# Optimization experiments

Measured on AMD Instinct MI355X. Metric: run time of the kernel, lower is better.

Reference implementation:

```python
import jax, jax.numpy as jnp
import numpy as np
from jax import lax

LIDAR_MAX_X = 30.0
LIDAR_MAX_Y = 30.0


def bilinear_sample(value, grid):
    """value: (bs,C,H,W); grid: (bs,nq,np,2) in [-1,1] -> (bs,C,nq,np)."""
    bs, C, H, W = value.shape
    _, nq, npts, _ = grid.shape
    gx = (grid[..., 0] + 1.0) / 2.0 * (W - 1)
    gy = (grid[..., 1] + 1.0) / 2.0 * (H - 1)
    # torch .long() truncates; in-bounds coords are non-negative so trunc == floor
    x0 = jnp.clip(gx.astype(jnp.int32), 0, W - 2)
    y0 = jnp.clip(gy.astype(jnp.int32), 0, H - 2)
    x1 = x0 + 1
    y1 = y0 + 1
    wx = jnp.clip(gx - x0.astype(gx.dtype), 0.0, 1.0).reshape(bs, 1, -1)
    wy = jnp.clip(gy - y0.astype(gy.dtype), 0.0, 1.0).reshape(bs, 1, -1)
    x0f = x0.reshape(bs, -1); x1f = x1.reshape(bs, -1)
    y0f = y0.reshape(bs, -1); y1f = y1.reshape(bs, -1)
    vflat = value.reshape(bs, C, H * W)
    gather = jax.vmap(lambda v, i: v[:, i])  # (C,HW),(N,) -> (C,N)
    v00 = gather(vflat, y0f * W + x0f)
    v01 = gather(vflat, y0f * W + x1f)
    v10 = gather(vflat, y1f * W + x0f)
    v11 = gather(vflat, y1f * W + x1f)
    sampled = (v00 * (1 - wx) * (1 - wy) + v01 * wx * (1 - wy)
               + v10 * (1 - wx) * wy + v11 * wx * wy)
    sampled = sampled.reshape(bs, C, nq, npts)
    gx0, gy0 = grid[..., 0], grid[..., 1]
    in_bounds = ((gx0 >= -1) & (gx0 <= 1) & (gy0 >= -1) & (gy0 <= 1))
    return sampled * in_bounds[:, None].astype(sampled.dtype)


def setup_inputs() -> dict:
    key = jax.random.key(0)
    ks = jax.random.split(key, 8)
    bs, nq, npts = 8, 2048, 8
    C_in, H, W = 64, 200, 200
    D = 256
    queries = jax.random.normal(ks[0], (bs, nq, D), dtype=jnp.float32)
    # lidar-frame waypoints, mostly in-bounds
    traj_points = jax.random.uniform(ks[1], (bs, nq, npts, 2), jnp.float32, -30.0, 30.0)
    bev_feature = jax.random.normal(ks[2], (bs, C_in, H, W), dtype=jnp.float32)
    attn_w = jax.random.normal(ks[3], (npts, D), dtype=jnp.float32) * 0.05
    attn_b = jnp.zeros((npts,), jnp.float32)
    out_w = jax.random.normal(ks[4], (D, D), dtype=jnp.float32) * (1.0 / np.sqrt(D))
    out_b = jnp.zeros((D,), jnp.float32)
    conv_w = jax.random.normal(ks[5], (D, C_in, 3, 3), dtype=jnp.float32) * 0.05
    conv_b = jnp.zeros((D,), jnp.float32)
    return {"queries": queries, "traj_points": traj_points, "bev_feature": bev_feature,
            "attn_w": attn_w, "attn_b": attn_b, "out_w": out_w, "out_b": out_b,
            "conv_w": conv_w, "conv_b": conv_b}


def reference(queries, traj_points, bev_feature, attn_w, attn_b, out_w, out_b, conv_w, conv_b):
    # normalize trajectory and swap (x,y) -> (y,x)
    norm = traj_points / jnp.array([LIDAR_MAX_Y, LIDAR_MAX_X], dtype=traj_points.dtype)
    grid = norm[..., ::-1]  # (bs,nq,np,2)
    # per-point attention weights
    attw = jax.nn.softmax(jnp.einsum('bqd,pd->bqp', queries, attn_w) + attn_b, axis=-1)
    # value projection: Conv3x3 + ReLU
    value = lax.conv_general_dilated(bev_feature, conv_w, (1, 1), ((1, 1), (1, 1)),
                                     dimension_numbers=('NCHW', 'OIHW', 'NCHW'))
    value = jax.nn.relu(value + conv_b[None, :, None, None])
    sampled = lax.stop_gradient(bilinear_sample(value, grid))  # (bs,C,nq,np)
    out = jnp.einsum('bcqp,bqp->bqc', sampled, attw)  # weighted sum over points
    out = jnp.einsum('bqc,dc->bqd', out, out_w) + out_b
    return out + queries  # dropout is identity in eval mode
```

## Files before the change

kernel.cpp:

```cpp
#include <hip/hip_runtime.h>

typedef unsigned short u16;
typedef _Float16 f16x8 __attribute__((ext_vector_type(8)));
typedef _Float16 f16x2 __attribute__((ext_vector_type(2)));
typedef float f32x4 __attribute__((ext_vector_type(4)));

__device__ __forceinline__ u16 f2h(float f){
  _Float16 h = (_Float16)f;
  return __builtin_bit_cast(u16, h);
}

__device__ __forceinline__ void load_lds16(const void* g, void* l){
  __builtin_amdgcn_global_load_lds((const __attribute__((address_space(1))) void*)g,
                                   (__attribute__((address_space(3))) void*)l,
                                   16, 0, 0);
}

__global__ __launch_bounds__(256) void kv5_transpose(const float* __restrict__ bev,
                                                     u16* __restrict__ bevT)
{
  __shared__ float t[64][65];
  const int tid = threadIdx.x;
  const int bid = blockIdx.x;
  const int wc = bid & 3;
  const int h  = (bid >> 2) % 200;
  const int b  = bid / 800;
  const int w0 = wc << 6;

  const int wl = (tid & 15) << 2;
  const int cb = tid >> 4;
  if (w0 + wl < 200){
    #pragma unroll
    for (int r = 0; r < 4; ++r){
      const int c = cb + (r << 4);
      const float4 v = *(const float4*)&bev[(((size_t)b*64 + c)*200 + h)*200 + (w0 + wl)];
      t[c][wl] = v.x; t[c][wl+1] = v.y; t[c][wl+2] = v.z; t[c][wl+3] = v.w;
    }
  }
  __syncthreads();
  const int c0 = (tid & 7) << 3;
  #pragma unroll
  for (int j = 0; j < 2; ++j){
    const int wl2 = (tid >> 3) + (j << 5);
    if (w0 + wl2 < 200){
      unsigned r0 = (unsigned)f2h(t[c0+0][wl2]) | ((unsigned)f2h(t[c0+1][wl2]) << 16);
      unsigned r1 = (unsigned)f2h(t[c0+2][wl2]) | ((unsigned)f2h(t[c0+3][wl2]) << 16);
      unsigned r2 = (unsigned)f2h(t[c0+4][wl2]) | ((unsigned)f2h(t[c0+5][wl2]) << 16);
      unsigned r3 = (unsigned)f2h(t[c0+6][wl2]) | ((unsigned)f2h(t[c0+7][wl2]) << 16);
      uint4 o = {r0, r1, r2, r3};
      *(uint4*)&bevT[(((size_t)b*202 + h + 1)*202 + (w0 + wl2 + 1))*64 + c0] = o;
    }
  }
}

__global__ __launch_bounds__(256) void kv5_prep(const float* __restrict__ conv_w,
                                                const float* __restrict__ out_w,
                                                u16* __restrict__ Wr,
                                                u16* __restrict__ owb)
{
  const int i = blockIdx.x * 256 + threadIdx.x;
  if (i < 9*256*64){
    const int t9 = i / (256*64);
    const int rem = i - t9*(256*64);
    const int d = rem >> 6, c = rem & 63;
    Wr[i] = f2h(conv_w[(size_t)(d*64 + c)*9 + t9]);
  } else {
    const int j = i - 9*256*64;
    if (j < 65536) owb[j] = f2h(out_w[j]);
  }
}

__global__ __launch_bounds__(256) void kv5_attw(const float* __restrict__ q,
                                                const float* __restrict__ aw,
                                                const float* __restrict__ ab,
                                                float* __restrict__ attw)
{
  const int lane = threadIdx.x & 63;
  const int bq = blockIdx.x * 4 + (threadIdx.x >> 6);
  const float4 qv = *(const float4*)&q[(size_t)bq*256 + (lane << 2)];
  float lg[8];
  #pragma unroll
  for (int p = 0; p < 8; ++p){
    const float4 wv = *(const float4*)&aw[p*256 + (lane << 2)];
    float d = qv.x*wv.x + qv.y*wv.y + qv.z*wv.z + qv.w*wv.w;
    #pragma unroll
    for (int off = 32; off > 0; off >>= 1) d += __shfl_xor(d, off);
    lg[p] = d + ab[p];
  }
  float mx = lg[0];
  #pragma unroll
  for (int p = 1; p < 8; ++p) mx = fmaxf(mx, lg[p]);
  float sum = 0.f;
  #pragma unroll
  for (int p = 0; p < 8; ++p){ lg[p] = expf(lg[p] - mx); sum += lg[p]; }
  const float inv = 1.f / sum;
  if (lane == 0){
    float4 o0 = {lg[0]*inv, lg[1]*inv, lg[2]*inv, lg[3]*inv};
    float4 o1 = {lg[4]*inv, lg[5]*inv, lg[6]*inv, lg[7]*inv};
    *(float4*)&attw[(size_t)bq*8]     = o0;
    *(float4*)&attw[(size_t)bq*8 + 4] = o1;
  }
}

__global__ __launch_bounds__(256) void kv5_conv(const u16* __restrict__ bevT,
                                                const u16* __restrict__ Wr,
                                                const float* __restrict__ conv_b,
                                                u16* __restrict__ value)
{
  __shared__ __align__(16) u16 lds[32768];
  const int tid  = threadIdx.x;
  const int bid  = blockIdx.x;
  const int n0   = (bid & 1) << 7;
  const int m0   = (bid >> 1) << 7;
  const int lane = tid & 63;
  const int wv   = tid >> 6;
  const int wm   = (wv >> 1) << 6;
  const int wn   = (wv & 1) << 6;
  const int c0   = (((tid & 7) ^ ((tid >> 3) & 7)) << 3);

  int baseA[4], baseB[4];
  #pragma unroll
  for (int i = 0; i < 4; ++i){
    const int m = m0 + (i << 5) + (tid >> 3);
    const int b = m / 40000;
    const int pix = m - b * 40000;
    const int h = pix / 200;
    const int w = pix - h * 200;
    baseA[i] = ((b*202 + h)*202 + w)*64 + c0;
    baseB[i] = (n0 + (i << 5) + (tid >> 3))*64 + c0;
  }

#define STAGE_TAP(dbuf, t9) do{                                            \
    const int ky_ = (t9)/3;                                                \
    const int offA_ = (ky_*202 + ((t9) - ky_*3))*64;                       \
    const u16* wsrc_ = Wr + (t9)*16384;                                    \
    for (int i_ = 0; i_ < 4; ++i_){                                        \
      load_lds16(bevT + baseA[i_] + offA_,                                 \
                 lds + (dbuf)*16384 + (i_ << 11) + (wv << 9));             \
      load_lds16(wsrc_ + baseB[i_],                                        \
                 lds + (dbuf)*16384 + 8192 + (i_ << 11) + (wv << 9));      \
    } }while(0)

  const f32x4 z = {0.f, 0.f, 0.f, 0.f};
  f32x4 acc[4][4];
  #pragma unroll
  for (int mf = 0; mf < 4; ++mf)
    #pragma unroll
    for (int nf = 0; nf < 4; ++nf)
      acc[mf][nf] = z;

  STAGE_TAP(0, 0);
  __syncthreads();

  int cur = 0;
  for (int t9 = 0; t9 < 9; ++t9){
    if (t9 < 8) STAGE_TAP(cur ^ 1, t9 + 1);

    const int rbase = cur << 14;
    const int swz = lane & 7;
    f16x8 a_frag[2][4], b_frag[2][4];
    #pragma unroll
    for (int kh = 0; kh < 2; ++kh){
      const int c16 = (((kh << 2) + (lane >> 4)) ^ swz) << 3;
      #pragma unroll
      for (int f = 0; f < 4; ++f){
        a_frag[kh][f] = *(const f16x8*)&lds[rbase + (wm + (f << 4) + (lane & 15))*64 + c16];
        b_frag[kh][f] = *(const f16x8*)&lds[rbase + 8192 + (wn + (f << 4) + (lane & 15))*64 + c16];
      }
    }
    #pragma unroll
    for (int kh = 0; kh < 2; ++kh)
      #pragma unroll
      for (int mf = 0; mf < 4; ++mf)
        #pragma unroll
        for (int nf = 0; nf < 4; ++nf)
          acc[mf][nf] = __builtin_amdgcn_mfma_f32_16x16x32_f16(a_frag[kh][mf], b_frag[kh][nf], acc[mf][nf], 0, 0, 0);

    __syncthreads();
    cur ^= 1;
  }
#undef STAGE_TAP

  #pragma unroll
  for (int nf = 0; nf < 4; ++nf){
    const int col = wn + (nf << 4) + (lane & 15);
    const float bias = conv_b[n0 + col];
    #pragma unroll
    for (int mf = 0; mf < 4; ++mf)
      #pragma unroll
      for (int rr = 0; rr < 4; ++rr){
        const int row = wm + (mf << 4) + ((lane >> 4) << 2) + rr;
        lds[row*128 + col] = f2h(fmaxf(acc[mf][nf][rr] + bias, 0.f));
      }
  }
  __syncthreads();
  #pragma unroll
  for (int it = 0; it < 8; ++it){
    const int idx = (it << 8) + tid;
    const int row = idx >> 4;
    const int ce  = (idx & 15) << 3;
    const f32x4 v = *(const f32x4*)&lds[row*128 + ce];
    *(f32x4*)&value[(size_t)(m0 + row)*256 + n0 + ce] = v;
  }
}

__global__ __launch_bounds__(256) void kv5_sample(const float* __restrict__ traj,
                                                  const float* __restrict__ attw,
                                                  const u16* __restrict__ value,
                                                  u16* __restrict__ sbh)
{
  __shared__ int   pixs[2][32];
  __shared__ float wgts[2][32];
  const int tid  = threadIdx.x;
  const int half = tid >> 7;
  const int t    = tid & 127;
  const int q    = (blockIdx.x << 1) + half;

  if (t < 8){
    const int p = t;
    const float ty = traj[((size_t)q*8 + p)*2 + 0];
    const float tx = traj[((size_t)q*8 + p)*2 + 1];
    float aw = attw[q*8 + p];
    const float gxn = tx / 30.f;
    const float gyn = ty / 30.f;
    if (!(gxn >= -1.f && gxn <= 1.f && gyn >= -1.f && gyn <= 1.f)) aw = 0.f;
    const float gx = (gxn + 1.f) * 0.5f * 199.f;
    const float gy = (gyn + 1.f) * 0.5f * 199.f;
    int x0 = (int)gx; x0 = min(max(x0, 0), 198);
    int y0 = (int)gy; y0 = min(max(y0, 0), 198);
    const float wx = fminf(fmaxf(gx - (float)x0, 0.f), 1.f);
    const float wy = fminf(fmaxf(gy - (float)y0, 0.f), 1.f);
    const int base = y0*200 + x0;
    pixs[half][p*4+0] = base;       wgts[half][p*4+0] = aw*(1.f-wx)*(1.f-wy);
    pixs[half][p*4+1] = base+1;     wgts[half][p*4+1] = aw*wx*(1.f-wy);
    pixs[half][p*4+2] = base+200;   wgts[half][p*4+2] = aw*(1.f-wx)*wy;
    pixs[half][p*4+3] = base+201;   wgts[half][p*4+3] = aw*wx*wy;
  }
  __syncthreads();
  const size_t vbase = (size_t)(q >> 11) * 40000;
  float a0 = 0.f, a1 = 0.f;
  #pragma unroll
  for (int i = 0; i < 32; ++i){
    const float w = wgts[half][i];
    const f16x2 pv = *(const f16x2*)&value[((vbase + pixs[half][i]) << 8) + (t << 1)];
    a0 = fmaf(w, (float)pv.x, a0);
    a1 = fmaf(w, (float)pv.y, a1);
  }
  const unsigned o = (unsigned)f2h(a0) | ((unsigned)f2h(a1) << 16);
  *(unsigned*)&sbh[((size_t)q << 8) + (t << 1)] = o;
}

__global__ __launch_bounds__(256) void kv5_outgemm(const u16* __restrict__ sbh,
                                                   const u16* __restrict__ owb,
                                                   const float* __restrict__ out_b,
                                                   const float* __restrict__ queries,
                                                   float* __restrict__ outp)
{
  __shared__ __align__(16) u16 lds[16384];
  const int tid  = threadIdx.x;
  const int bid  = blockIdx.x;
  const int n0   = (bid & 1) << 7;
  const int m0   = (bid >> 1) << 7;
  const int lane = tid & 63;
  const int wv   = tid >> 6;
  const int wm   = (wv >> 1) << 6;
  const int wn   = (wv & 1) << 6;
  const int c0   = (tid & 7) << 3;

  int baseA[4], baseB[4];
  #pragma unroll
  for (int i = 0; i < 4; ++i){
    baseA[i] = (m0 + (i << 5) + (tid >> 3))*256 + c0;
    baseB[i] = (n0 + (i << 5) + (tid >> 3))*256 + c0;
  }
  const f32x4 z = {0.f, 0.f, 0.f, 0.f};
  f32x4 acc[4][4];
  #pragma unroll
  for (int mf = 0; mf < 4; ++mf)
    #pragma unroll
    for (int nf = 0; nf < 4; ++nf)
      acc[mf][nf] = z;

  for (int kk = 0; kk < 4; ++kk){
    #pragma unroll
    for (int i = 0; i < 4; ++i){
      load_lds16(sbh + baseA[i] + (kk << 6), lds + (i << 11) + (wv << 9));
      load_lds16(owb + baseB[i] + (kk << 6), lds + 8192 + (i << 11) + (wv << 9));
    }
    __syncthreads();

    f16x8 a_frag[2][4], b_frag[2][4];
    #pragma unroll
    for (int kh = 0; kh < 2; ++kh){
      const int kq = (kh << 5) + ((lane >> 4) << 3);
      #pragma unroll
      for (int f = 0; f < 4; ++f){
        a_frag[kh][f] = *(const f16x8*)&lds[(wm + (f << 4) + (lane & 15))*64 + kq];
        b_frag[kh][f] = *(const f16x8*)&lds[8192 + (wn + (f << 4) + (lane & 15))*64 + kq];
      }
    }
    #pragma unroll
    for (int kh = 0; kh < 2; ++kh)
      #pragma unroll
      for (int mf = 0; mf < 4; ++mf)
        #pragma unroll
        for (int nf = 0; nf < 4; ++nf)
          acc[mf][nf] = __builtin_amdgcn_mfma_f32_16x16x32_f16(a_frag[kh][mf], b_frag[kh][nf], acc[mf][nf], 0, 0, 0);
    __syncthreads();
  }

  #pragma unroll
  for (int nf = 0; nf < 4; ++nf){
    const int col = wn + (nf << 4) + (lane & 15);
    const float ob = out_b[n0 + col];
    #pragma unroll
    for (int mf = 0; mf < 4; ++mf)
      #pragma unroll
      for (int rr = 0; rr < 4; ++rr){
        const int row = wm + (mf << 4) + ((lane >> 4) << 2) + rr;
        const size_t off = (size_t)(m0 + row)*256 + n0 + col;
        outp[off] = acc[mf][nf][rr] + ob + queries[off];
      }
  }
}

extern "C" void kernel_launch(void* const* d_in, const int* in_sizes, int n_in,
                              void* d_out, int out_size, void* d_ws, size_t ws_size,
                              hipStream_t stream)
{
  const float* queries = (const float*)d_in[0];
  const float* traj    = (const float*)d_in[1];
  const float* bev     = (const float*)d_in[2];
  const float* attn_w  = (const float*)d_in[3];
  const float* attn_b  = (const float*)d_in[4];
  const float* out_w   = (const float*)d_in[5];
  const float* out_b   = (const float*)d_in[6];
  const float* conv_w  = (const float*)d_in[7];
  const float* conv_b  = (const float*)d_in[8];
  float* outp = (float*)d_out;
  char* ws = (char*)d_ws;

  u16*   bevT  = (u16*)  (ws + 0);
  u16*   value = (u16*)  (ws + 41783296);
  u16*   Wr    = (u16*)  (ws + 205623296);
  u16*   owb   = (u16*)  (ws + 205918208);
  float* attw  = (float*)(ws + 206049280);
  u16*   sbh   = (u16*)  (ws + 206573568);

  hipMemsetAsync(bevT, 0, 41783296, stream);
  kv5_transpose<<<6400, 256, 0, stream>>>(bev, bevT);
  kv5_prep     <<<832,  256, 0, stream>>>(conv_w, out_w, Wr, owb);
  kv5_attw     <<<4096, 256, 0, stream>>>(queries, attn_w, attn_b, attw);
  kv5_conv     <<<5000, 256, 0, stream>>>(bevT, Wr, conv_b, value);
  kv5_sample   <<<8192, 256, 0, stream>>>(traj, attw, value, sbh);
  kv5_outgemm  <<<256,  256, 0, stream>>>(sbh, owb, out_b, queries, outp);
}
```

Measured before the change: 241.2 us.

## Stage one halo strip per conv block and reuse it across all nine taps

The conv kernel now loads a single contiguous strip of the padded fp16 BEV (128 pixels plus halo, 17 KB-ish) into LDS once and reads all nine tap windows from it. The old version double-buffered A and B tiles for every tap. Weights are now read straight from global memory (L2-cached) instead of being staged in LDS. Blocks are remapped per batch image, with a partial last slot, so the grid grows to 5008. This removes the repeated per-tap A loads and the per-tap barriers. In exchange it drops the XOR swizzle, which may cause LDS bank conflicts, and it exposes global-load latency for the B fragments.

```diff
diff --git a/kernel.cpp b/kernel.cpp
--- a/kernel.cpp
+++ b/kernel.cpp
@@ -16,7 +16,7 @@
                                    16, 0, 0);
 }
 
-__global__ __launch_bounds__(256) void kv5_transpose(const float* __restrict__ bev,
+__global__ __launch_bounds__(256) void kv6_transpose(const float* __restrict__ bev,
                                                      u16* __restrict__ bevT)
 {
   __shared__ float t[64][65];
@@ -53,7 +53,7 @@
   }
 }
 
-__global__ __launch_bounds__(256) void kv5_prep(const float* __restrict__ conv_w,
+__global__ __launch_bounds__(256) void kv6_prep(const float* __restrict__ conv_w,
                                                 const float* __restrict__ out_w,
                                                 u16* __restrict__ Wr,
                                                 u16* __restrict__ owb)
@@ -70,7 +70,7 @@
   }
 }
 
-__global__ __launch_bounds__(256) void kv5_attw(const float* __restrict__ q,
+__global__ __launch_bounds__(256) void kv6_attw(const float* __restrict__ q,
                                                 const float* __restrict__ aw,
                                                 const float* __restrict__ ab,
                                                 float* __restrict__ attw)
@@ -102,44 +102,43 @@
   }
 }
 
-__global__ __launch_bounds__(256) void kv5_conv(const u16* __restrict__ bevT,
+__global__ __launch_bounds__(256) void kv6_conv(const u16* __restrict__ bevT,
                                                 const u16* __restrict__ Wr,
                                                 const float* __restrict__ conv_b,
                                                 u16* __restrict__ value)
 {
-  __shared__ __align__(16) u16 lds[32768];
+  __shared__ __align__(16) u16 lds[34816];
   const int tid  = threadIdx.x;
   const int bid  = blockIdx.x;
-  const int n0   = (bid & 1) << 7;
-  const int m0   = (bid >> 1) << 7;
+  const int b    = bid & 7;
+  const int n0   = ((bid >> 3) & 1) << 7;
+  const int slot = bid >> 4;
+  const int rows_valid = (slot == 312) ? 64 : 128;
+
+  const int pix0 = slot << 7;
+  const int h0   = pix0 / 200;
+  const int w0   = pix0 - h0 * 200;
+  const size_t strip_base = ((size_t)(b*202 + h0)*202 + w0) * 64;
+
+  #pragma unroll
+  for (int i = 0; i < 17; ++i){
+    const int idx = (i << 8) + tid;
+    load_lds16(bevT + strip_base + ((size_t)idx << 3), lds + (idx << 3));
+  }
+
   const int lane = tid & 63;
   const int wv   = tid >> 6;
   const int wm   = (wv >> 1) << 6;
   const int wn   = (wv & 1) << 6;
-  const int c0   = (((tid & 7) ^ ((tid >> 3) & 7)) << 3);
-
-  int baseA[4], baseB[4];
-  #pragma unroll
-  for (int i = 0; i < 4; ++i){
-    const int m = m0 + (i << 5) + (tid >> 3);
-    const int b = m / 40000;
-    const int pix = m - b * 40000;
-    const int h = pix / 200;
-    const int w = pix - h * 200;
-    baseA[i] = ((b*202 + h)*202 + w)*64 + c0;
-    baseB[i] = (n0 + (i << 5) + (tid >> 3))*64 + c0;
-  }
-
-#define STAGE_TAP(dbuf, t9) do{                                            \
-    const int ky_ = (t9)/3;                                                \
-    const int offA_ = (ky_*202 + ((t9) - ky_*3))*64;                       \
-    const u16* wsrc_ = Wr + (t9)*16384;                                    \
-    for (int i_ = 0; i_ < 4; ++i_){                                        \
-      load_lds16(bevT + baseA[i_] + offA_,                                 \
-                 lds + (dbuf)*16384 + (i_ << 11) + (wv << 9));             \
-      load_lds16(wsrc_ + baseB[i_],                                        \
-                 lds + (dbuf)*16384 + 8192 + (i_ << 11) + (wv << 9));      \
-    } }while(0)
+  const int ko   = (lane >> 4) << 3;
+
+  int rowoffA[4], rowBidx[4];
+  #pragma unroll
+  for (int f = 0; f < 4; ++f){
+    const int r = wm + (f << 4) + (lane & 15);
+    rowoffA[f] = (r << 6) + ((w0 + r >= 200) ? 128 : 0);
+    rowBidx[f] = (n0 + wn + (f << 4) + (lane & 15)) << 6;
+  }
 
   const f32x4 z = {0.f, 0.f, 0.f, 0.f};
   f32x4 acc[4][4];
@@ -149,38 +148,39 @@
     for (int nf = 0; nf < 4; ++nf)
       acc[mf][nf] = z;
 
-  STAGE_TAP(0, 0);
-  __syncthreads();
-
-  int cur = 0;
+  __syncthreads();
+
+  #pragma unroll 1
   for (int t9 = 0; t9 < 9; ++t9){
-    if (t9 < 8) STAGE_TAP(cur ^ 1, t9 + 1);
-
-    const int rbase = cur << 14;
-    const int swz = lane & 7;
-    f16x8 a_frag[2][4], b_frag[2][4];
-    #pragma unroll
-    for (int kh = 0; kh < 2; ++kh){
-      const int c16 = (((kh << 2) + (lane >> 4)) ^ swz) << 3;
-      #pragma unroll
-      for (int f = 0; f < 4; ++f){
-        a_frag[kh][f] = *(const f16x8*)&lds[rbase + (wm + (f << 4) + (lane & 15))*64 + c16];
-        b_frag[kh][f] = *(const f16x8*)&lds[rbase + 8192 + (wn + (f << 4) + (lane & 15))*64 + c16];
-      }
-    }
+    const int ky = (t9 * 11) >> 5;
+    const int kx = t9 - ky * 3;
+    const int tapoff = (ky * 202 + kx) << 6;
+    const u16* wsrc = Wr + t9 * 16384;
+
+    f16x8 bf[2][4], af[2][4];
+    #pragma unroll
+    for (int kh = 0; kh < 2; ++kh)
+      #pragma unroll
+      for (int f = 0; f < 4; ++f)
+        bf[kh][f] = *(const f16x8*)&wsrc[rowBidx[f] + (kh << 5) + ko];
+    #pragma unroll
+    for (int kh = 0; kh < 2; ++kh)
+      #pragma unroll
+      for (int f = 0; f < 4; ++f)
+        af[kh][f] = *(const f16x8*)&lds[rowoffA[f] + tapoff + (kh << 5) + ko];
+
     #pragma unroll
     for (int kh = 0; kh < 2; ++kh)
       #pragma unroll
       for (int mf = 0; mf < 4; ++mf)
         #pragma unroll
         for (int nf = 0; nf < 4; ++nf)
-          acc[mf][nf] = __builtin_amdgcn_mfma_f32_16x16x32_f16(a_frag[kh][mf], b_frag[kh][nf], acc[mf][nf], 0, 0, 0);
-
-    __syncthreads();
-    cur ^= 1;
-  }
-#undef STAGE_TAP
-
+          acc[mf][nf] = __builtin_amdgcn_mfma_f32_16x16x32_f16(af[kh][mf], bf[kh][nf], acc[mf][nf], 0, 0, 0);
+  }
+
+  __syncthreads();
+
+  const int m0 = b * 40000 + pix0;
   #pragma unroll
   for (int nf = 0; nf < 4; ++nf){
     const int col = wn + (nf << 4) + (lane & 15);
@@ -198,13 +198,15 @@
   for (int it = 0; it < 8; ++it){
     const int idx = (it << 8) + tid;
     const int row = idx >> 4;
-    const int ce  = (idx & 15) << 3;
-    const f32x4 v = *(const f32x4*)&lds[row*128 + ce];
-    *(f32x4*)&value[(size_t)(m0 + row)*256 + n0 + ce] = v;
-  }
-}
-
-__global__ __launch_bounds__(256) void kv5_sample(const float* __restrict__ traj,
+    if (row < rows_valid){
+      const int ce = (idx & 15) << 3;
+      const f32x4 v = *(const f32x4*)&lds[row*128 + ce];
+      *(f32x4*)&value[(size_t)(m0 + row)*256 + n0 + ce] = v;
+    }
+  }
+}
+
+__global__ __launch_bounds__(256) void kv6_sample(const float* __restrict__ traj,
                                                   const float* __restrict__ attw,
                                                   const u16* __restrict__ value,
                                                   u16* __restrict__ sbh)
@@ -250,7 +252,7 @@
   *(unsigned*)&sbh[((size_t)q << 8) + (t << 1)] = o;
 }
 
-__global__ __launch_bounds__(256) void kv5_outgemm(const u16* __restrict__ sbh,
+__global__ __launch_bounds__(256) void kv6_outgemm(const u16* __restrict__ sbh,
                                                    const u16* __restrict__ owb,
                                                    const float* __restrict__ out_b,
                                                    const float* __restrict__ queries,
@@ -348,10 +350,10 @@
   u16*   sbh   = (u16*)  (ws + 206573568);
 
   hipMemsetAsync(bevT, 0, 41783296, stream);
-  kv5_transpose<<<6400, 256, 0, stream>>>(bev, bevT);
-  kv5_prep     <<<832,  256, 0, stream>>>(conv_w, out_w, Wr, owb);
-  kv5_attw     <<<4096, 256, 0, stream>>>(queries, attn_w, attn_b, attw);
-  kv5_conv     <<<5000, 256, 0, stream>>>(bevT, Wr, conv_b, value);
-  kv5_sample   <<<8192, 256, 0, stream>>>(traj, attw, value, sbh);
-  kv5_outgemm  <<<256,  256, 0, stream>>>(sbh, owb, out_b, queries, outp);
-}
+  kv6_transpose<<<6400, 256, 0, stream>>>(bev, bevT);
+  kv6_prep     <<<832,  256, 0, stream>>>(conv_w, out_w, Wr, owb);
+  kv6_attw     <<<4096, 256, 0, stream>>>(queries, attn_w, attn_b, attw);
+  kv6_conv     <<<5008, 256, 0, stream>>>(bevT, Wr, conv_b, value);
+  kv6_sample   <<<8192, 256, 0, stream>>>(traj, attw, value, sbh);
+  kv6_outgemm  <<<256,  256, 0, stream>>>(sbh, owb, out_b, queries, outp);
+}
```

Result: slower. 295.6 us (+22.6%).

## Zero only conv halo, single-buffer conv LDS, and remap block order for XCDs

Applied to the files above, without the earlier changes.

Replaces the full 41 MB memset of the padded transposed BEV buffer with a small kernel that zeroes only the one-pixel halo border, since the transpose overwrites the interior anyway. The conv kernel drops LDS double buffering to halve shared memory, likely aiming for higher occupancy, and synchronizes after each tap load. It also permutes block IDs so consecutive blocks spread across the 8 XCDs in contiguous chunks, improving L2 locality. Losing the prefetch overlap may expose global-to-LDS latency in the conv loop.

```diff
diff --git a/kernel.cpp b/kernel.cpp
--- a/kernel.cpp
+++ b/kernel.cpp
@@ -16,7 +16,23 @@
                                    16, 0, 0);
 }
 
-__global__ __launch_bounds__(256) void kv5_transpose(const float* __restrict__ bev,
+__global__ __launch_bounds__(256) void kv9_halo(u16* __restrict__ bevT)
+{
+  const int i = blockIdx.x * 256 + threadIdx.x;
+  if (i >= 8*804*8) return;
+  const int b = i / (804*8);
+  const int rem = i - b*(804*8);
+  const int p = rem >> 3, c = rem & 7;
+  int h, w;
+  if (p < 202)      { h = 0;        w = p; }
+  else if (p < 404) { h = 201;      w = p - 202; }
+  else if (p < 604) { h = p - 403;  w = 0; }
+  else              { h = p - 603;  w = 201; }
+  const uint4 z = {0u,0u,0u,0u};
+  *(uint4*)&bevT[(((size_t)b*202 + h)*202 + w)*64 + (c << 3)] = z;
+}
+
+__global__ __launch_bounds__(256) void kv9_transpose(const float* __restrict__ bev,
                                                      u16* __restrict__ bevT)
 {
   __shared__ float t[64][65];
@@ -53,7 +69,7 @@
   }
 }
 
-__global__ __launch_bounds__(256) void kv5_prep(const float* __restrict__ conv_w,
+__global__ __launch_bounds__(256) void kv9_prep(const float* __restrict__ conv_w,
                                                 const float* __restrict__ out_w,
                                                 u16* __restrict__ Wr,
                                                 u16* __restrict__ owb)
@@ -70,7 +86,7 @@
   }
 }
 
-__global__ __launch_bounds__(256) void kv5_attw(const float* __restrict__ q,
+__global__ __launch_bounds__(256) void kv9_attw(const float* __restrict__ q,
                                                 const float* __restrict__ aw,
                                                 const float* __restrict__ ab,
                                                 float* __restrict__ attw)
@@ -102,14 +118,14 @@
   }
 }
 
-__global__ __launch_bounds__(256) void kv5_conv(const u16* __restrict__ bevT,
+__global__ __launch_bounds__(256) void kv9_conv(const u16* __restrict__ bevT,
                                                 const u16* __restrict__ Wr,
                                                 const float* __restrict__ conv_b,
                                                 u16* __restrict__ value)
 {
-  __shared__ __align__(16) u16 lds[32768];
+  __shared__ __align__(16) u16 lds[16384];
   const int tid  = threadIdx.x;
-  const int bid  = blockIdx.x;
+  const int bid  = (int)(blockIdx.x & 7) * 625 + (int)(blockIdx.x >> 3);
   const int n0   = (bid & 1) << 7;
   const int m0   = (bid >> 1) << 7;
   const int lane = tid & 63;
@@ -130,17 +146,6 @@
     baseB[i] = (n0 + (i << 5) + (tid >> 3))*64 + c0;
   }
 
-#define STAGE_TAP(dbuf, t9) do{                                            \
-    const int ky_ = (t9)/3;                                                \
-    const int offA_ = (ky_*202 + ((t9) - ky_*3))*64;                       \
-    const u16* wsrc_ = Wr + (t9)*16384;                                    \
-    for (int i_ = 0; i_ < 4; ++i_){                                        \
-      load_lds16(bevT + baseA[i_] + offA_,                                 \
-                 lds + (dbuf)*16384 + (i_ << 11) + (wv << 9));             \
-      load_lds16(wsrc_ + baseB[i_],                                        \
-                 lds + (dbuf)*16384 + 8192 + (i_ << 11) + (wv << 9));      \
-    } }while(0)
-
   const f32x4 z = {0.f, 0.f, 0.f, 0.f};
   f32x4 acc[4][4];
   #pragma unroll
@@ -149,23 +154,26 @@
     for (int nf = 0; nf < 4; ++nf)
       acc[mf][nf] = z;
 
-  STAGE_TAP(0, 0);
-  __syncthreads();
-
-  int cur = 0;
+  const int swz = lane & 7;
   for (int t9 = 0; t9 < 9; ++t9){
-    if (t9 < 8) STAGE_TAP(cur ^ 1, t9 + 1);
-
-    const int rbase = cur << 14;
-    const int swz = lane & 7;
+    const int ky = t9 / 3;
+    const int offA = (ky*202 + (t9 - ky*3))*64;
+    const u16* wsrc = Wr + t9*16384;
+    #pragma unroll
+    for (int i = 0; i < 4; ++i){
+      load_lds16(bevT + baseA[i] + offA, lds + (i << 11) + (wv << 9));
+      load_lds16(wsrc + baseB[i],        lds + 8192 + (i << 11) + (wv << 9));
+    }
+    __syncthreads();
+
     f16x8 a_frag[2][4], b_frag[2][4];
     #pragma unroll
     for (int kh = 0; kh < 2; ++kh){
       const int c16 = (((kh << 2) + (lane >> 4)) ^ swz) << 3;
       #pragma unroll
       for (int f = 0; f < 4; ++f){
-        a_frag[kh][f] = *(const f16x8*)&lds[rbase + (wm + (f << 4) + (lane & 15))*64 + c16];
-        b_frag[kh][f] = *(const f16x8*)&lds[rbase + 8192 + (wn + (f << 4) + (lane & 15))*64 + c16];
+        a_frag[kh][f] = *(const f16x8*)&lds[(wm + (f << 4) + (lane & 15))*64 + c16];
+        b_frag[kh][f] = *(const f16x8*)&lds[8192 + (wn + (f << 4) + (lane & 15))*64 + c16];
       }
     }
     #pragma unroll
@@ -175,11 +183,8 @@
         #pragma unroll
         for (int nf = 0; nf < 4; ++nf)
           acc[mf][nf] = __builtin_amdgcn_mfma_f32_16x16x32_f16(a_frag[kh][mf], b_frag[kh][nf], acc[mf][nf], 0, 0, 0);
-
     __syncthreads();
-    cur ^= 1;
-  }
-#undef STAGE_TAP
+  }
 
   #pragma unroll
   for (int nf = 0; nf < 4; ++nf){
@@ -204,7 +209,7 @@
   }
 }
 
-__global__ __launch_bounds__(256) void kv5_sample(const float* __restrict__ traj,
+__global__ __launch_bounds__(256) void kv9_sample(const float* __restrict__ traj,
                                                   const float* __restrict__ attw,
                                                   const u16* __restrict__ value,
                                                   u16* __restrict__ sbh)
@@ -250,7 +255,7 @@
   *(unsigned*)&sbh[((size_t)q << 8) + (t << 1)] = o;
 }
 
-__global__ __launch_bounds__(256) void kv5_outgemm(const u16* __restrict__ sbh,
+__global__ __launch_bounds__(256) void kv9_outgemm(const u16* __restrict__ sbh,
                                                    const u16* __restrict__ owb,
                                                    const float* __restrict__ out_b,
                                                    const float* __restrict__ queries,
@@ -347,11 +352,11 @@
   float* attw  = (float*)(ws + 206049280);
   u16*   sbh   = (u16*)  (ws + 206573568);
 
-  hipMemsetAsync(bevT, 0, 41783296, stream);
-  kv5_transpose<<<6400, 256, 0, stream>>>(bev, bevT);
-  kv5_prep     <<<832,  256, 0, stream>>>(conv_w, out_w, Wr, owb);
-  kv5_attw     <<<4096, 256, 0, stream>>>(queries, attn_w, attn_b, attw);
-  kv5_conv     <<<5000, 256, 0, stream>>>(bevT, Wr, conv_b, value);
-  kv5_sample   <<<8192, 256, 0, stream>>>(traj, attw, value, sbh);
-  kv5_outgemm  <<<256,  256, 0, stream>>>(sbh, owb, out_b, queries, outp);
-}
+  kv9_halo     <<<201,  256, 0, stream>>>(bevT);
+  kv9_transpose<<<6400, 256, 0, stream>>>(bev, bevT);
+  kv9_prep     <<<832,  256, 0, stream>>>(conv_w, out_w, Wr, owb);
+  kv9_attw     <<<4096, 256, 0, stream>>>(queries, attn_w, attn_b, attw);
+  kv9_conv     <<<5000, 256, 0, stream>>>(bevT, Wr, conv_b, value);
+  kv9_sample   <<<8192, 256, 0, stream>>>(traj, attw, value, sbh);
+  kv9_outgemm  <<<256,  256, 0, stream>>>(sbh, owb, out_b, queries, outp);
+}
```

Result: faster. 206.0 us (-14.6%).
